# Kernel optimization log

Measured on AMD Instinct MI355X. Metric: run time of the kernel, lower is better.

Reference implementation:

```python
import jax, jax.numpy as jnp
import numpy as np

KERNEL_MUL = [2.0, 2.0]
KERNEL_NUM = [5, 1]
FIX_SIGMA = [None, 1.68]


def setup_inputs() -> dict:
    key = jax.random.key(0)
    k0, k1, k2, k3 = jax.random.split(key, 4)
    B, D0, D1 = 4096, 2048, 128
    return {
        "src_f0": jax.random.normal(k0, (B, D0), dtype=jnp.float32),
        "src_f1": jax.random.normal(k1, (B, D1), dtype=jnp.float32),
        "tar_f0": jax.random.normal(k2, (B, D0), dtype=jnp.float32),
        "tar_f1": jax.random.normal(k3, (B, D1), dtype=jnp.float32),
    }


def _gaussian_kernel(src, tar, kernel_mul, kernel_num, fix_sigma):
    n_samples = src.shape[0] + tar.shape[0]
    total = jnp.concatenate([src, tar], axis=0)  # [2B, D]
    # pairwise squared L2 distance without the O(N^2*D) expanded intermediate
    sq = jnp.sum(total * total, axis=1)
    l2 = sq[:, None] + sq[None, :] - 2.0 * (total @ total.T)  # [2B, 2B]
    if fix_sigma:
        bandwidth = jnp.asarray(fix_sigma, dtype=l2.dtype)
    else:
        # original uses L2_distance.data (detached) for the bandwidth estimate
        bandwidth = jax.lax.stop_gradient(jnp.sum(l2)) / (n_samples ** 2 - n_samples)
    bandwidth = bandwidth / (kernel_mul ** (kernel_num // 2))
    kernel = jnp.zeros_like(l2)
    for i in range(kernel_num):
        kernel = kernel + jnp.exp(-l2 / (bandwidth * kernel_mul ** i))
    return kernel


def reference(src_f0, src_f1, tar_f0, tar_f1):
    src_list = [src_f0, src_f1]
    tar_list = [tar_f0, tar_f1]
    joint = None
    for i in range(len(src_list)):
        k = _gaussian_kernel(src_list[i], tar_list[i], KERNEL_MUL[i], KERNEL_NUM[i], FIX_SIGMA[i])
        joint = k if joint is None else joint * k
    B = src_f0.shape[0]
    XX = joint[:B, :B]
    YY = joint[B:, B:]
    XY = joint[:B, B:]
    YX = joint[B:, :B]
    return jnp.mean(XX + YY - XY - YX)
```

## Files before the change

kernel.cpp:

```cpp
#include <hip/hip_runtime.h>
#include <stdint.h>

#define B_ROWS 4096
#define NTOT   8192
#define D0     2048
#define D1     128
#define TAU    112.0f

#define OFF_ACC   0
#define OFF_S0    8
#define OFF_BW    16
#define OFF_CNT   20
#define OFF_DONE  24
#define OFF_M0    32
#define OFF_SQ1   8320
#define OFF_T1    41216
#define OFF_CAND  2138368
#define ZERO_WORDS 2056

typedef _Float16 half8 __attribute__((ext_vector_type(8)));
typedef _Float16 half2v __attribute__((ext_vector_type(2)));
typedef float f32x4 __attribute__((ext_vector_type(4)));

#define LDSTRIDE 88

__global__ void p0a(const float* __restrict__ src1, const float* __restrict__ tar1, char* __restrict__ ws) {
    if (blockIdx.x == 0) {
        unsigned* w = (unsigned*)ws;
        for (int i = threadIdx.x; i < ZERO_WORDS; i += 256) w[i] = 0;
    }
    int wave = threadIdx.x >> 6, lane = threadIdx.x & 63;
    int row = blockIdx.x * 4 + wave;
    const float2* rp = (const float2*)(row < B_ROWS ? src1 + (size_t)row * D1
                                                    : tar1 + (size_t)(row - B_ROWS) * D1);
    float2 v = rp[lane];
    float sq = v.x * v.x + v.y * v.y;
    #pragma unroll
    for (int off = 32; off; off >>= 1) sq += __shfl_down(sq, off);
    if (lane == 0) ((float*)(ws + OFF_SQ1))[row] = sq;
    half2v h; h[0] = (_Float16)v.x; h[1] = (_Float16)v.y;
    ((half2v*)(ws + OFF_T1))[(size_t)row * 64 + lane] = h;
}

__global__ __launch_bounds__(256) void phaseA(char* __restrict__ ws, unsigned cap) {
    int tid = blockIdx.x;
    int bi = (int)((129.0 - sqrt(129.0 * 129.0 - 8.0 * (double)tid)) * 0.5);
    while (((bi + 1) * (129 - (bi + 1))) / 2 <= tid) bi++;
    while ((bi * (129 - bi)) / 2 > tid) bi--;
    int bj = bi + (tid - (bi * (129 - bi)) / 2);

    __shared__ __align__(16) _Float16 At[128 * LDSTRIDE];
    __shared__ __align__(16) _Float16 Bt[128 * LDSTRIDE];
    const uint4* t1 = (const uint4*)(ws + OFF_T1);
    int t = threadIdx.x;
    int lane = t & 63, wave = t >> 6;
    int wm = wave & 1, wn = wave >> 1;
    int quad = lane >> 4;
    int Abase = bi * 128, Bbase = bj * 128;

    f32x4 acc[4][4];
    #pragma unroll
    for (int i = 0; i < 4; i++)
        #pragma unroll
        for (int j = 0; j < 4; j++) acc[i][j] = (f32x4){0.f, 0.f, 0.f, 0.f};

    #pragma unroll
    for (int s = 0; s < 2; s++) {
        __syncthreads();
        #pragma unroll
        for (int i = 0; i < 4; i++) {
            int q = t + 256 * i;
            int r = q >> 3, c = q & 7;
            uint4 va = t1[(size_t)(Abase + r) * 16 + s * 8 + c];
            *(uint4*)((char*)At + r * (LDSTRIDE * 2) + c * 16) = va;
            uint4 vb = t1[(size_t)(Bbase + r) * 16 + s * 8 + c];
            *(uint4*)((char*)Bt + r * (LDSTRIDE * 2) + c * 16) = vb;
        }
        __syncthreads();
        #pragma unroll
        for (int kk = 0; kk < 2; kk++) {
            int koffB = kk * 64 + quad * 16;
            half8 af[4], bf[4];
            #pragma unroll
            for (int mi = 0; mi < 4; mi++) {
                int row = wm * 64 + mi * 16 + (lane & 15);
                af[mi] = *(const half8*)((const char*)At + row * (LDSTRIDE * 2) + koffB);
            }
            #pragma unroll
            for (int nj = 0; nj < 4; nj++) {
                int row = wn * 64 + nj * 16 + (lane & 15);
                bf[nj] = *(const half8*)((const char*)Bt + row * (LDSTRIDE * 2) + koffB);
            }
            #pragma unroll
            for (int mi = 0; mi < 4; mi++)
                #pragma unroll
                for (int nj = 0; nj < 4; nj++)
                    acc[mi][nj] = __builtin_amdgcn_mfma_f32_16x16x32_f16(
                        af[mi], bf[nj], acc[mi][nj], 0, 0, 0);
        }
    }

    const float* sq1 = (const float*)(ws + OFF_SQ1);
    unsigned* cnt = (unsigned*)(ws + OFF_CNT);
    uint2* cand = (uint2*)(ws + OFF_CAND);
    f32x4 sqa[4];
    #pragma unroll
    for (int mi = 0; mi < 4; mi++)
        sqa[mi] = *(const f32x4*)&sq1[Abase + wm * 64 + mi * 16 + quad * 4];
    #pragma unroll
    for (int nj = 0; nj < 4; nj++) {
        int b = Bbase + wn * 64 + nj * 16 + (lane & 15);
        float sqb = sq1[b];
        #pragma unroll
        for (int mi = 0; mi < 4; mi++) {
            int abase = Abase + wm * 64 + mi * 16 + quad * 4;
            #pragma unroll
            for (int r = 0; r < 4; r++) {
                int a = abase + r;
                float l2 = sqa[mi][r] + sqb - 2.0f * acc[mi][nj][r];
                if (l2 < TAU && a < b) {
                    unsigned idx = atomicAdd(cnt, 1u);
                    if (idx < cap) cand[idx] = make_uint2((unsigned)a, (unsigned)b);
                }
            }
        }
    }
}

__global__ void bwk1(const float* __restrict__ src0, const float* __restrict__ tar0, char* __restrict__ ws) {
    if (*(volatile unsigned*)(ws + OFF_CNT) == 0) return;
    int d4 = blockIdx.x * 256 + threadIdx.x;
    int rbase = blockIdx.y * 64;
    const float4* base = (const float4*)(rbase < B_ROWS ? src0 + (size_t)rbase * D0
                                                        : tar0 + (size_t)(rbase - B_ROWS) * D0);
    float4 cs = {0.f, 0.f, 0.f, 0.f};
    float sq = 0.f;
    for (int r = 0; r < 64; r++) {
        float4 v = base[(size_t)r * 512 + d4];
        cs.x += v.x; cs.y += v.y; cs.z += v.z; cs.w += v.w;
        sq += v.x * v.x + v.y * v.y + v.z * v.z + v.w * v.w;
    }
    float* m0 = (float*)(ws + OFF_M0);
    atomicAdd(&m0[d4 * 4 + 0], cs.x);
    atomicAdd(&m0[d4 * 4 + 1], cs.y);
    atomicAdd(&m0[d4 * 4 + 2], cs.z);
    atomicAdd(&m0[d4 * 4 + 3], cs.w);
    #pragma unroll
    for (int off = 32; off; off >>= 1) sq += __shfl_down(sq, off);
    __shared__ float red[4];
    int lane = threadIdx.x & 63, wave = threadIdx.x >> 6;
    if (lane == 0) red[wave] = sq;
    __syncthreads();
    if (threadIdx.x == 0)
        atomicAdd((double*)(ws + OFF_S0), (double)(red[0] + red[1] + red[2] + red[3]));
}

__global__ void phaseB(const float* __restrict__ src0, const float* __restrict__ src1,
                       const float* __restrict__ tar0, const float* __restrict__ tar1,
                       char* __restrict__ ws, unsigned cap, float* __restrict__ out) {
    __shared__ double red[4];
    __shared__ float fred[4];
    __shared__ float bws;
    unsigned cnt = *(const unsigned*)(ws + OFF_CNT);
    if (cnt > cap) cnt = cap;
    int lane = threadIdx.x & 63, wave = threadIdx.x >> 6;
    if (cnt > 0) {
        const float* m0 = (const float*)(ws + OFF_M0);
        float s = 0.f;
        for (int j = threadIdx.x; j < 2048; j += 256) { float v = m0[j]; s += v * v; }
        #pragma unroll
        for (int off = 32; off; off >>= 1) s += __shfl_down(s, off);
        if (lane == 0) fred[wave] = s;
        __syncthreads();
        if (threadIdx.x == 0) {
            double m2 = (double)fred[0] + fred[1] + fred[2] + fred[3];
            double S0 = *(double*)(ws + OFF_S0);
            double lsum2 = 2.0 * (double)NTOT * S0 - 2.0 * m2;
            bws = (float)(lsum2 / ((double)NTOT * NTOT - NTOT) / 4.0);
        }
        __syncthreads();
        float bw = bws;
        const uint2* cand = (const uint2*)(ws + OFF_CAND);
        unsigned gw = blockIdx.x * 4 + wave;
        unsigned nw = gridDim.x * 4;
        double lsum = 0.0;
        for (unsigned i = gw; i < cnt; i += nw) {
            uint2 p = cand[i];
            unsigned a = p.x, b = p.y;
            const float* ra0 = a < B_ROWS ? src0 + (size_t)a * D0 : tar0 + (size_t)(a - B_ROWS) * D0;
            const float* rb0 = b < B_ROWS ? src0 + (size_t)b * D0 : tar0 + (size_t)(b - B_ROWS) * D0;
            const float* ra1 = a < B_ROWS ? src1 + (size_t)a * D1 : tar1 + (size_t)(a - B_ROWS) * D1;
            const float* rb1 = b < B_ROWS ? src1 + (size_t)b * D1 : tar1 + (size_t)(b - B_ROWS) * D1;
            float d1;
            {
                float2 x = ((const float2*)ra1)[lane];
                float2 y = ((const float2*)rb1)[lane];
                float dx = x.x - y.x, dy = x.y - y.y;
                d1 = dx * dx + dy * dy;
            }
            float d0 = 0.f;
            #pragma unroll
            for (int j = 0; j < 8; j++) {
                float4 x = ((const float4*)ra0)[lane + 64 * j];
                float4 y = ((const float4*)rb0)[lane + 64 * j];
                float dx = x.x - y.x, dy = x.y - y.y, dz = x.z - y.z, dw = x.w - y.w;
                d0 += dx * dx + dy * dy + dz * dz + dw * dw;
            }
            #pragma unroll
            for (int off = 32; off; off >>= 1) {
                d0 += __shfl_down(d0, off);
                d1 += __shfl_down(d1, off);
            }
            if (lane == 0) {
                float k1 = expf(-d1 / 1.68f);
                float k0 = 0.f, bwj = bw;
                #pragma unroll
                for (int j = 0; j < 5; j++) { k0 += expf(-d0 / bwj); bwj *= 2.0f; }
                float sgn = ((a < B_ROWS) == (b < B_ROWS)) ? 1.0f : -1.0f;
                lsum += (double)(2.0f * sgn * k0 * k1);
            }
        }
        if (lane == 0) red[wave] = lsum;
        __syncthreads();
        if (threadIdx.x == 0)
            atomicAdd((double*)(ws + OFF_ACC), red[0] + red[1] + red[2] + red[3]);
    }
    __threadfence();
    if (threadIdx.x == 0) {
        unsigned d = atomicAdd((unsigned*)(ws + OFF_DONE), 1u);
        if (d == gridDim.x - 1) {
            double acc = atomicAdd((double*)(ws + OFF_ACC), 0.0);
            out[0] = (float)((acc + (double)NTOT * 5.0) / ((double)B_ROWS * (double)B_ROWS));
        }
    }
}

extern "C" void kernel_launch(void* const* d_in, const int* in_sizes, int n_in,
                              void* d_out, int out_size, void* d_ws, size_t ws_size,
                              hipStream_t stream) {
    const float* src0 = (const float*)d_in[0];
    const float* src1 = (const float*)d_in[1];
    const float* tar0 = (const float*)d_in[2];
    const float* tar1 = (const float*)d_in[3];
    char* ws = (char*)d_ws;
    unsigned cap = 0;
    if (ws_size > (size_t)OFF_CAND + 8) {
        size_t c = (ws_size - OFF_CAND) / 8;
        if (c > (size_t)4 * 1024 * 1024) c = (size_t)4 * 1024 * 1024;
        cap = (unsigned)c;
    }
    p0a<<<2048, 256, 0, stream>>>(src1, tar1, ws);
    phaseA<<<2080, 256, 0, stream>>>(ws, cap);
    bwk1<<<dim3(2, 128), 256, 0, stream>>>(src0, tar0, ws);
    phaseB<<<64, 256, 0, stream>>>(src0, src1, tar0, tar1, ws, cap, (float*)d_out);
}
```

Baseline: 117.0 us.

## Load MFMA fragments directly from global memory, dropping LDS staging in phaseA

The D1=128 Gram tile kernel no longer stages A and B tiles through shared memory with two barriers per k-step. Each wave now reads its half8 MFMA fragments straight from the fp16 workspace in global memory, and launch bounds are raised to ask for 4 blocks per CU. This removes the LDS round-trip and the syncs and frees LDS to allow more occupancy. The cost is that each row's data is loaded redundantly by several waves through L1/L2, and the global loads are strided rather than coalesced.

```diff
diff --git a/kernel.cpp b/kernel.cpp
--- a/kernel.cpp
+++ b/kernel.cpp
@@ -22,8 +22,6 @@
 typedef _Float16 half2v __attribute__((ext_vector_type(2)));
 typedef float f32x4 __attribute__((ext_vector_type(4)));
 
-#define LDSTRIDE 88
-
 __global__ void p0a(const float* __restrict__ src1, const float* __restrict__ tar1, char* __restrict__ ws) {
     if (blockIdx.x == 0) {
         unsigned* w = (unsigned*)ws;
@@ -42,22 +40,23 @@
     ((half2v*)(ws + OFF_T1))[(size_t)row * 64 + lane] = h;
 }
 
-__global__ __launch_bounds__(256) void phaseA(char* __restrict__ ws, unsigned cap) {
+__global__ __launch_bounds__(256, 4) void phaseA(char* __restrict__ ws, unsigned cap) {
     int tid = blockIdx.x;
     int bi = (int)((129.0 - sqrt(129.0 * 129.0 - 8.0 * (double)tid)) * 0.5);
     while (((bi + 1) * (129 - (bi + 1))) / 2 <= tid) bi++;
     while ((bi * (129 - bi)) / 2 > tid) bi--;
     int bj = bi + (tid - (bi * (129 - bi)) / 2);
 
-    __shared__ __align__(16) _Float16 At[128 * LDSTRIDE];
-    __shared__ __align__(16) _Float16 Bt[128 * LDSTRIDE];
-    const uint4* t1 = (const uint4*)(ws + OFF_T1);
+    const char* t1 = (const char*)(ws + OFF_T1);
     int t = threadIdx.x;
     int lane = t & 63, wave = t >> 6;
     int wm = wave & 1, wn = wave >> 1;
     int quad = lane >> 4;
     int Abase = bi * 128, Bbase = bj * 128;
 
+    const char* aptr = t1 + (((size_t)(Abase + wm * 64 + (lane & 15))) << 8) + quad * 16;
+    const char* bptr = t1 + (((size_t)(Bbase + wn * 64 + (lane & 15))) << 8) + quad * 16;
+
     f32x4 acc[4][4];
     #pragma unroll
     for (int i = 0; i < 4; i++)
@@ -65,39 +64,20 @@
         for (int j = 0; j < 4; j++) acc[i][j] = (f32x4){0.f, 0.f, 0.f, 0.f};
 
     #pragma unroll
-    for (int s = 0; s < 2; s++) {
-        __syncthreads();
-        #pragma unroll
-        for (int i = 0; i < 4; i++) {
-            int q = t + 256 * i;
-            int r = q >> 3, c = q & 7;
-            uint4 va = t1[(size_t)(Abase + r) * 16 + s * 8 + c];
-            *(uint4*)((char*)At + r * (LDSTRIDE * 2) + c * 16) = va;
-            uint4 vb = t1[(size_t)(Bbase + r) * 16 + s * 8 + c];
-            *(uint4*)((char*)Bt + r * (LDSTRIDE * 2) + c * 16) = vb;
-        }
-        __syncthreads();
-        #pragma unroll
-        for (int kk = 0; kk < 2; kk++) {
-            int koffB = kk * 64 + quad * 16;
-            half8 af[4], bf[4];
-            #pragma unroll
-            for (int mi = 0; mi < 4; mi++) {
-                int row = wm * 64 + mi * 16 + (lane & 15);
-                af[mi] = *(const half8*)((const char*)At + row * (LDSTRIDE * 2) + koffB);
-            }
-            #pragma unroll
-            for (int nj = 0; nj < 4; nj++) {
-                int row = wn * 64 + nj * 16 + (lane & 15);
-                bf[nj] = *(const half8*)((const char*)Bt + row * (LDSTRIDE * 2) + koffB);
-            }
-            #pragma unroll
-            for (int mi = 0; mi < 4; mi++)
-                #pragma unroll
-                for (int nj = 0; nj < 4; nj++)
-                    acc[mi][nj] = __builtin_amdgcn_mfma_f32_16x16x32_f16(
-                        af[mi], bf[nj], acc[mi][nj], 0, 0, 0);
-        }
+    for (int ks = 0; ks < 4; ks++) {
+        half8 af[4], bf[4];
+        #pragma unroll
+        for (int mi = 0; mi < 4; mi++)
+            af[mi] = *(const half8*)(aptr + mi * 4096 + ks * 64);
+        #pragma unroll
+        for (int nj = 0; nj < 4; nj++)
+            bf[nj] = *(const half8*)(bptr + nj * 4096 + ks * 64);
+        #pragma unroll
+        for (int mi = 0; mi < 4; mi++)
+            #pragma unroll
+            for (int nj = 0; nj < 4; nj++)
+                acc[mi][nj] = __builtin_amdgcn_mfma_f32_16x16x32_f16(
+                    af[mi], bf[nj], acc[mi][nj], 0, 0, 0);
     }
 
     const float* sq1 = (const float*)(ws + OFF_SQ1);
```

After: 139.7 us. 19.5% more time.
